# Kernel optimization log

Hardware: AMD Instinct MI355X
Metric: run time of the kernel (lower is better)

The kernel has to match this reference:

```python
import jax, jax.numpy as jnp
import numpy as np

EMBED_DIM = 1024
SEQ_LEN = 2048
BATCH = 4


def setup_inputs() -> dict:
    key = jax.random.key(0)
    kx, kq, kk, kv = jax.random.split(key, 4)
    scale = 1.0 / np.sqrt(EMBED_DIM)
    x = jax.random.normal(kx, (BATCH, SEQ_LEN, EMBED_DIM), dtype=jnp.float32)
    # nn.Linear weights are [out, in]; stored transposed-application here
    W_query = jax.random.normal(kq, (EMBED_DIM, EMBED_DIM), dtype=jnp.float32) * scale
    W_key = jax.random.normal(kk, (EMBED_DIM, EMBED_DIM), dtype=jnp.float32) * scale
    W_value = jax.random.normal(kv, (EMBED_DIM, EMBED_DIM), dtype=jnp.float32) * scale
    return {"x": x, "W_query": W_query, "W_key": W_key, "W_value": W_value}


def reference(x, W_query, W_key, W_value):
    # x: [B, S, D]; W_*: [D_out, D_in] (torch nn.Linear layout -> y = x @ W.T)
    B, S, D = x.shape
    q = jnp.einsum("bsd,ed->bse", x, W_query)
    k = jnp.einsum("bsd,ed->bse", x, W_key)
    v = jnp.einsum("bsd,ed->bse", x, W_value)
    scores = jnp.einsum("bqd,bkd->bqk", q, k)  # [B, S, S]
    causal = jnp.triu(jnp.ones((S, S), dtype=bool), k=1)  # True above diagonal
    scores = jnp.where(causal, -jnp.inf, scores)
    weights = jax.nn.softmax(scores / jnp.sqrt(jnp.asarray(D, x.dtype)), axis=-1)
    return jnp.einsum("bqk,bkd->bqd", weights, v)
```

## Files before the change

### kernel.cpp

```cpp
#include <hip/hip_runtime.h>
#include <stdint.h>

typedef __bf16 bf16_t;
typedef __bf16 bf16x8 __attribute__((ext_vector_type(8)));
typedef float  f32x4  __attribute__((ext_vector_type(4)));

#define AS1 __attribute__((address_space(1)))
#define AS3 __attribute__((address_space(3)))

__device__ __forceinline__ void gld_lds16(const bf16_t* g, void* s) {
  __builtin_amdgcn_global_load_lds((const AS1 uint32_t*)g, (AS3 uint32_t*)s, 16, 0, 0);
}

__global__ __launch_bounds__(256) void convert_all_kernel(
    const float* __restrict__ X,  const float* __restrict__ Wq,
    const float* __restrict__ Wk, const float* __restrict__ Wv,
    bf16_t* __restrict__ Xc, bf16_t* __restrict__ Wqc,
    bf16_t* __restrict__ Wkc, bf16_t* __restrict__ Wvc) {
  const int blk = blockIdx.x;
  const float* src; bf16_t* dst; int base;
  if (blk < 4096)      { src = X;  dst = Xc;  base = 0;    }
  else if (blk < 4608) { src = Wq; dst = Wqc; base = 4096; }
  else if (blk < 5120) { src = Wk; dst = Wkc; base = 4608; }
  else                 { src = Wv; dst = Wvc; base = 5120; }
  const int i = ((blk - base) * 256 + threadIdx.x) * 8;
  const float4 a = ((const float4*)(src + i))[0];
  const float4 b = ((const float4*)(src + i))[1];
  bf16x8 v;
  v[0] = (bf16_t)a.x; v[1] = (bf16_t)a.y; v[2] = (bf16_t)a.z; v[3] = (bf16_t)a.w;
  v[4] = (bf16_t)b.x; v[5] = (bf16_t)b.y; v[6] = (bf16_t)b.z; v[7] = (bf16_t)b.w;
  *(bf16x8*)(dst + i) = v;
}

__device__ __forceinline__ void gemm_bt_core(
    const bf16_t* __restrict__ A, int lda,
    const bf16_t* __restrict__ B, int ldb,
    int m0, int n0, int kBeg, int kEnd,
    bf16_t* As, bf16_t* Bs, f32x4 acc[4][4])
{
  const int tid  = threadIdx.x;
  const int lane = tid & 63;
  const int wave = tid >> 6;
  const int wm = (wave >> 1) * 64;
  const int wn = (wave & 1) * 64;
  const int fr = lane & 15;
  const int ck = lane >> 4;

  const int off0 = wave * 2048 + lane * 16;
  const int row0 = wave * 32 + (lane >> 2);
  const int row1 = row0 + 16;
  const int kg   = ((lane & 3) ^ ((row0 >> 1) & 3)) * 8;

  int aoff[4], boff[4];
#pragma unroll
  for (int i = 0; i < 4; ++i) {
    const int ra = wm + i * 16 + fr;
    const int rb = wn + i * 16 + fr;
    aoff[i] = ra * 64 + ((ck ^ ((ra >> 1) & 3)) * 16);
    boff[i] = rb * 64 + ((ck ^ ((rb >> 1) & 3)) * 16);
  }

  for (int kt = kBeg; kt < kEnd; kt += 32) {
    __syncthreads();
    gld_lds16(A + (size_t)(m0 + row0) * lda + kt + kg, (char*)As + off0);
    gld_lds16(A + (size_t)(m0 + row1) * lda + kt + kg, (char*)As + off0 + 1024);
    gld_lds16(B + (size_t)(n0 + row0) * ldb + kt + kg, (char*)Bs + off0);
    gld_lds16(B + (size_t)(n0 + row1) * ldb + kt + kg, (char*)Bs + off0 + 1024);
    __syncthreads();

    bf16x8 af[4], bfv[4];
#pragma unroll
    for (int mi = 0; mi < 4; ++mi)
      af[mi] = *(const bf16x8*)((char*)As + aoff[mi]);
#pragma unroll
    for (int ni = 0; ni < 4; ++ni)
      bfv[ni] = *(const bf16x8*)((char*)Bs + boff[ni]);
#pragma unroll
    for (int mi = 0; mi < 4; ++mi)
#pragma unroll
      for (int ni = 0; ni < 4; ++ni)
        acc[mi][ni] = __builtin_amdgcn_mfma_f32_16x16x32_bf16(
            af[mi], bfv[ni], acc[mi][ni], 0, 0, 0);
  }
}

__device__ __forceinline__ void gemm64_core(
    const bf16_t* __restrict__ A, int lda,
    const bf16_t* __restrict__ B, int ldb,
    int m0, int n0, int kBeg, int kEnd,
    bf16_t* As, bf16_t* Bs, f32x4 acc[2][2])
{
  const int lane = threadIdx.x & 63;
  const int wave = threadIdx.x >> 6;
  const int wm = (wave >> 1) * 32;
  const int wn = (wave & 1) * 32;
  const int fr = lane & 15;
  const int ck = lane >> 4;

  const int off0 = wave * 1024 + lane * 16;
  const int row0 = wave * 16 + (lane >> 2);
  const int kg   = ((lane & 3) ^ ((row0 >> 1) & 3)) * 8;

  int aoff[2], boff[2];
#pragma unroll
  for (int i = 0; i < 2; ++i) {
    const int ra = wm + i * 16 + fr;
    const int rb = wn + i * 16 + fr;
    aoff[i] = ra * 64 + ((ck ^ ((ra >> 1) & 3)) * 16);
    boff[i] = rb * 64 + ((ck ^ ((rb >> 1) & 3)) * 16);
  }

  for (int kt = kBeg; kt < kEnd; kt += 32) {
    __syncthreads();
    gld_lds16(A + (size_t)(m0 + row0) * lda + kt + kg, (char*)As + off0);
    gld_lds16(B + (size_t)(n0 + row0) * ldb + kt + kg, (char*)Bs + off0);
    __syncthreads();

    bf16x8 af[2], bfv[2];
#pragma unroll
    for (int mi = 0; mi < 2; ++mi)
      af[mi] = *(const bf16x8*)((char*)As + aoff[mi]);
#pragma unroll
    for (int ni = 0; ni < 2; ++ni)
      bfv[ni] = *(const bf16x8*)((char*)Bs + boff[ni]);
#pragma unroll
    for (int mi = 0; mi < 2; ++mi)
#pragma unroll
      for (int ni = 0; ni < 2; ++ni)
        acc[mi][ni] = __builtin_amdgcn_mfma_f32_16x16x32_bf16(
            af[mi], bfv[ni], acc[mi][ni], 0, 0, 0);
  }
}

__device__ __forceinline__ void gemm64x128_core(
    const bf16_t* __restrict__ A, int lda,
    const bf16_t* __restrict__ B, int ldb,
    int m0, int n0, int kEnd,
    bf16_t* As, bf16_t* Bs, f32x4 acc[2][4])
{
  const int lane = threadIdx.x & 63;
  const int wave = threadIdx.x >> 6;
  const int wm = (wave >> 1) * 32;
  const int wn = (wave & 1) * 64;
  const int fr = lane & 15;
  const int ck = lane >> 4;

  const int off0 = wave * 1024 + lane * 16;
  const int row0 = wave * 16 + (lane >> 2);
  const int row1 = row0 + 64;
  const int kg   = ((lane & 3) ^ ((row0 >> 1) & 3)) * 8;

  int aoff[2], boff[4];
#pragma unroll
  for (int i = 0; i < 2; ++i) {
    const int ra = wm + i * 16 + fr;
    aoff[i] = ra * 64 + ((ck ^ ((ra >> 1) & 3)) * 16);
  }
#pragma unroll
  for (int i = 0; i < 4; ++i) {
    const int rb = wn + i * 16 + fr;
    boff[i] = rb * 64 + ((ck ^ ((rb >> 1) & 3)) * 16);
  }

  for (int kt = 0; kt < kEnd; kt += 32) {
    __syncthreads();
    gld_lds16(A + (size_t)(m0 + row0) * lda + kt + kg, (char*)As + off0);
    gld_lds16(B + (size_t)(n0 + row0) * ldb + kt + kg, (char*)Bs + off0);
    gld_lds16(B + (size_t)(n0 + row1) * ldb + kt + kg, (char*)Bs + off0 + 4096);
    __syncthreads();

    bf16x8 af[2], bfv[4];
#pragma unroll
    for (int mi = 0; mi < 2; ++mi)
      af[mi] = *(const bf16x8*)((char*)As + aoff[mi]);
#pragma unroll
    for (int ni = 0; ni < 4; ++ni)
      bfv[ni] = *(const bf16x8*)((char*)Bs + boff[ni]);
#pragma unroll
    for (int mi = 0; mi < 2; ++mi)
#pragma unroll
      for (int ni = 0; ni < 4; ++ni)
        acc[mi][ni] = __builtin_amdgcn_mfma_f32_16x16x32_bf16(
            af[mi], bfv[ni], acc[mi][ni], 0, 0, 0);
  }
}

__global__ __launch_bounds__(256) void qkv_kernel(
    const bf16_t* __restrict__ X,
    const bf16_t* __restrict__ Wq, const bf16_t* __restrict__ Wk,
    const bf16_t* __restrict__ Wv,
    bf16_t* __restrict__ Q, bf16_t* __restrict__ K, bf16_t* __restrict__ V)
{
  __shared__ bf16_t As[128 * 32];
  __shared__ bf16_t Bs[128 * 32];
  const int m0 = blockIdx.x * 128;
  const int n0 = blockIdx.y * 128;
  const int z  = blockIdx.z;
  const bf16_t* W = (z == 0) ? Wq : (z == 1) ? Wk : Wv;
  bf16_t* Out     = (z == 0) ? Q  : (z == 1) ? K  : V;

  f32x4 acc[4][4] = {};
  gemm_bt_core(X, 1024, W, 1024, m0, n0, 0, 1024, As, Bs, acc);

  const int lane = threadIdx.x & 63;
  const int wave = threadIdx.x >> 6;
  const int wm = (wave >> 1) * 64, wn = (wave & 1) * 64;
#pragma unroll
  for (int mi = 0; mi < 4; ++mi)
#pragma unroll
    for (int r = 0; r < 4; ++r) {
      const int row = m0 + wm + mi * 16 + (lane >> 4) * 4 + r;
#pragma unroll
      for (int ni = 0; ni < 4; ++ni) {
        const int col = n0 + wn + ni * 16 + (lane & 15);
        Out[(size_t)row * 1024 + col] = (bf16_t)acc[mi][ni][r];
      }
    }
}

__global__ __launch_bounds__(256) void vt_kernel(
    const bf16_t* __restrict__ V, bf16_t* __restrict__ Vt)
{
  __shared__ bf16_t t[64][66];
  const int b  = blockIdx.z;
  const int s0 = blockIdx.x * 64;
  const int d0 = blockIdx.y * 64;
  const bf16_t* Vb = V  + (size_t)b * 2048 * 1024;
  bf16_t* Vtb      = Vt + (size_t)b * 1024 * 2048;
  const int c = threadIdx.x & 63, r4 = threadIdx.x >> 6;
#pragma unroll
  for (int i = 0; i < 16; ++i) {
    const int r = r4 + i * 4;
    t[r][c] = Vb[(size_t)(s0 + r) * 1024 + d0 + c];
  }
  __syncthreads();
#pragma unroll
  for (int i = 0; i < 16; ++i) {
    const int r = r4 + i * 4;
    Vtb[(size_t)(d0 + r) * 2048 + s0 + c] = t[c][r];
  }
}

__global__ __launch_bounds__(256) void scores_exp_kernel(
    const bf16_t* __restrict__ Q, const bf16_t* __restrict__ K,
    bf16_t* __restrict__ P, float* __restrict__ partials, int b0)
{
  const int kt = blockIdx.x;
  const int m0 = blockIdx.y * 64;
  const int n0 = kt * 128;
  if (n0 > m0 + 63) return;
  __shared__ bf16_t As[64 * 32];
  __shared__ bf16_t Bs[128 * 32];
  __shared__ float rowsum[2][64];
  const int batch = b0 + blockIdx.z;
  const bf16_t* Qb = Q + (size_t)batch * 2048 * 1024;
  const bf16_t* Kb = K + (size_t)batch * 2048 * 1024;
  bf16_t* Pb = P + (size_t)blockIdx.z * 2048 * 2048;
  float* lp  = partials + ((size_t)blockIdx.z * 16 + kt) * 2048;

  f32x4 acc[2][4] = {};
  gemm64x128_core(Qb, 1024, Kb, 1024, m0, n0, 1024, As, Bs, acc);

  const int lane = threadIdx.x & 63;
  const int wave = threadIdx.x >> 6;
  const int wm = (wave >> 1) * 32, wn = (wave & 1) * 64;
  const float c = 0.04508422f;
#pragma unroll
  for (int mi = 0; mi < 2; ++mi)
#pragma unroll
    for (int r = 0; r < 4; ++r) {
      const int lrow = wm + mi * 16 + (lane >> 4) * 4 + r;
      const int row  = m0 + lrow;
      float rs = 0.f;
#pragma unroll
      for (int ni = 0; ni < 4; ++ni) {
        const int col = n0 + wn + ni * 16 + (lane & 15);
        float p = exp2f(acc[mi][ni][r] * c);
        if (col > row) p = 0.f;
        const bf16_t pb = (bf16_t)p;
        Pb[(size_t)row * 2048 + col] = pb;
        rs += (float)pb;
      }
      rs += __shfl_xor(rs, 1);
      rs += __shfl_xor(rs, 2);
      rs += __shfl_xor(rs, 4);
      rs += __shfl_xor(rs, 8);
      if ((lane & 15) == 0) rowsum[wave & 1][lrow] = rs;
    }
  __syncthreads();
  if (threadIdx.x < 64)
    lp[m0 + threadIdx.x] = rowsum[0][threadIdx.x] + rowsum[1][threadIdx.x];
}

__global__ __launch_bounds__(256) void pv_kernel(
    const bf16_t* __restrict__ P, const bf16_t* __restrict__ Vt,
    const float* __restrict__ partials, float* __restrict__ out, int b0)
{
  __shared__ bf16_t As[64 * 32];
  __shared__ bf16_t Bs[64 * 32];
  const int n0   = blockIdx.x * 64;
  const int pair = blockIdx.y;
  const int batch = b0 + blockIdx.z;
  const bf16_t* Pb  = P  + (size_t)blockIdx.z * 2048 * 2048;
  const bf16_t* Vtb = Vt + (size_t)batch * 1024 * 2048;
  const float* lp = partials + (size_t)blockIdx.z * 16 * 2048;
  float* ob = out + (size_t)batch * 2048 * 1024;

  const int lane = threadIdx.x & 63;
  const int wave = threadIdx.x >> 6;
  const int wm = (wave >> 1) * 32, wn = (wave & 1) * 32;

#pragma unroll
  for (int t = 0; t < 2; ++t) {
    const int mt = t ? (31 - pair) : pair;
    const int m0 = mt * 64;
    const int kEnd = m0 + 64;

    f32x4 acc[2][2] = {};
    gemm64_core(Pb, 2048, Vtb, 2048, m0, n0, 0, kEnd, As, Bs, acc);

#pragma unroll
    for (int mi = 0; mi < 2; ++mi)
#pragma unroll
      for (int r = 0; r < 4; ++r) {
        const int row = m0 + wm + mi * 16 + (lane >> 4) * 4 + r;
        const int tmax = row >> 7;
        float l = 0.f;
        for (int kt = 0; kt <= tmax; ++kt) l += lp[kt * 2048 + row];
        const float inv = 1.f / l;
#pragma unroll
        for (int ni = 0; ni < 2; ++ni) {
          const int col = n0 + wn + ni * 16 + (lane & 15);
          ob[(size_t)row * 1024 + col] = acc[mi][ni][r] * inv;
        }
      }
  }
}

extern "C" void kernel_launch(void* const* d_in, const int* in_sizes, int n_in,
                              void* d_out, int out_size, void* d_ws, size_t ws_size,
                              hipStream_t stream) {
  const float* X  = (const float*)d_in[0];
  const float* Wq = (const float*)d_in[1];
  const float* Wk = (const float*)d_in[2];
  const float* Wv = (const float*)d_in[3];
  float* out = (float*)d_out;
  char* ws = (char*)d_ws;

  const size_t NX = (size_t)4 * 2048 * 1024;
  const size_t NW = (size_t)1024 * 1024;
  const size_t QKV_BYTES = NX * 2;

  size_t  off  = 0;
  bf16_t* Xc   = (bf16_t*)(ws + off); off += NX * 2;
  bf16_t* Wqc  = (bf16_t*)(ws + off); off += NW * 2;
  bf16_t* Wkc  = (bf16_t*)(ws + off); off += NW * 2;
  bf16_t* Wvc  = (bf16_t*)(ws + off); off += NW * 2;
  bf16_t* Q    = (bf16_t*)(ws + off); off += QKV_BYTES;
  bf16_t* K    = (bf16_t*)(ws + off); off += QKV_BYTES;
  bf16_t* V    = (bf16_t*)(ws + off); off += QKV_BYTES;
  bf16_t* Vt   = (bf16_t*)(ws + off); off += QKV_BYTES;

  const size_t L_B = (size_t)16 * 2048 * 4;
  const size_t P_B = (size_t)2048 * 2048 * 2;
  const int NB = (ws_size >= off + 4 * (L_B + P_B)) ? 4 : 1;
  float*  Lp = (float*)(ws + off);
  bf16_t* Pb = (bf16_t*)(ws + off + (size_t)NB * L_B);

  convert_all_kernel<<<dim3(5632), 256, 0, stream>>>(X, Wq, Wk, Wv, Xc, Wqc, Wkc, Wvc);
  qkv_kernel<<<dim3(64, 8, 3), 256, 0, stream>>>(Xc, Wqc, Wkc, Wvc, Q, K, V);
  vt_kernel<<<dim3(32, 16, 4), 256, 0, stream>>>(V, Vt);
  for (int b0 = 0; b0 < 4; b0 += NB) {
    scores_exp_kernel<<<dim3(16, 32, NB), 256, 0, stream>>>(Q, K, Pb, Lp, b0);
    pv_kernel<<<dim3(16, 16, NB), 256, 0, stream>>>(Pb, Vt, Lp, out, b0);
  }
}
```

Measured before the change: 268.8 us.

## Use 128x128 tiles in PV GEMM and precompute inverse row sums

The PV kernel moves from 64x64 tiles with paired causal rows to 128x128 tiles using the existing gemm_bt_core, with a per-batch rotation of the row-tile order. A separate small kernel sums the per-tile partial row sums once and stores reciprocals in the reused Wqc buffer, so the epilogue no longer repeats the partial-sum loop in every block. Larger tiles raise data reuse and MFMA density per LDS load. The cost is that the causal work imbalance is no longer hidden by pairing, and there are fewer blocks plus one extra launch.

```diff
diff --git a/kernel.cpp b/kernel.cpp
--- a/kernel.cpp
+++ b/kernel.cpp
@@ -84,54 +84,6 @@
   }
 }
 
-__device__ __forceinline__ void gemm64_core(
-    const bf16_t* __restrict__ A, int lda,
-    const bf16_t* __restrict__ B, int ldb,
-    int m0, int n0, int kBeg, int kEnd,
-    bf16_t* As, bf16_t* Bs, f32x4 acc[2][2])
-{
-  const int lane = threadIdx.x & 63;
-  const int wave = threadIdx.x >> 6;
-  const int wm = (wave >> 1) * 32;
-  const int wn = (wave & 1) * 32;
-  const int fr = lane & 15;
-  const int ck = lane >> 4;
-
-  const int off0 = wave * 1024 + lane * 16;
-  const int row0 = wave * 16 + (lane >> 2);
-  const int kg   = ((lane & 3) ^ ((row0 >> 1) & 3)) * 8;
-
-  int aoff[2], boff[2];
-#pragma unroll
-  for (int i = 0; i < 2; ++i) {
-    const int ra = wm + i * 16 + fr;
-    const int rb = wn + i * 16 + fr;
-    aoff[i] = ra * 64 + ((ck ^ ((ra >> 1) & 3)) * 16);
-    boff[i] = rb * 64 + ((ck ^ ((rb >> 1) & 3)) * 16);
-  }
-
-  for (int kt = kBeg; kt < kEnd; kt += 32) {
-    __syncthreads();
-    gld_lds16(A + (size_t)(m0 + row0) * lda + kt + kg, (char*)As + off0);
-    gld_lds16(B + (size_t)(n0 + row0) * ldb + kt + kg, (char*)Bs + off0);
-    __syncthreads();
-
-    bf16x8 af[2], bfv[2];
-#pragma unroll
-    for (int mi = 0; mi < 2; ++mi)
-      af[mi] = *(const bf16x8*)((char*)As + aoff[mi]);
-#pragma unroll
-    for (int ni = 0; ni < 2; ++ni)
-      bfv[ni] = *(const bf16x8*)((char*)Bs + boff[ni]);
-#pragma unroll
-    for (int mi = 0; mi < 2; ++mi)
-#pragma unroll
-      for (int ni = 0; ni < 2; ++ni)
-        acc[mi][ni] = __builtin_amdgcn_mfma_f32_16x16x32_bf16(
-            af[mi], bfv[ni], acc[mi][ni], 0, 0, 0);
-  }
-}
-
 __device__ __forceinline__ void gemm64x128_core(
     const bf16_t* __restrict__ A, int lda,
     const bf16_t* __restrict__ B, int ldb,
@@ -292,49 +244,53 @@
     lp[m0 + threadIdx.x] = rowsum[0][threadIdx.x] + rowsum[1][threadIdx.x];
 }
 
+__global__ __launch_bounds__(256) void lsum_kernel(
+    const float* __restrict__ partials, float* __restrict__ Linv)
+{
+  const int id  = blockIdx.x * 256 + threadIdx.x;
+  const int z   = id >> 11;
+  const int row = id & 2047;
+  const float* lp = partials + (size_t)z * 16 * 2048;
+  const int tmax = row >> 7;
+  float l = 0.f;
+  for (int kt = 0; kt <= tmax; ++kt) l += lp[kt * 2048 + row];
+  Linv[id] = 1.f / l;
+}
+
 __global__ __launch_bounds__(256) void pv_kernel(
     const bf16_t* __restrict__ P, const bf16_t* __restrict__ Vt,
-    const float* __restrict__ partials, float* __restrict__ out, int b0)
-{
-  __shared__ bf16_t As[64 * 32];
-  __shared__ bf16_t Bs[64 * 32];
-  const int n0   = blockIdx.x * 64;
-  const int pair = blockIdx.y;
-  const int batch = b0 + blockIdx.z;
-  const bf16_t* Pb  = P  + (size_t)blockIdx.z * 2048 * 2048;
+    const float* __restrict__ Linv, float* __restrict__ out, int b0)
+{
+  __shared__ bf16_t As[128 * 32];
+  __shared__ bf16_t Bs[128 * 32];
+  const int zb = blockIdx.z;
+  const int mt = (blockIdx.y + 5 * zb) & 15;
+  const int m0 = mt * 128;
+  const int n0 = blockIdx.x * 128;
+  const int batch = b0 + zb;
+  const bf16_t* Pb  = P  + (size_t)zb * 2048 * 2048;
   const bf16_t* Vtb = Vt + (size_t)batch * 1024 * 2048;
-  const float* lp = partials + (size_t)blockIdx.z * 16 * 2048;
+  const float* li = Linv + (size_t)zb * 2048;
   float* ob = out + (size_t)batch * 2048 * 1024;
+
+  f32x4 acc[4][4] = {};
+  gemm_bt_core(Pb, 2048, Vtb, 2048, m0, n0, 0, m0 + 128, As, Bs, acc);
 
   const int lane = threadIdx.x & 63;
   const int wave = threadIdx.x >> 6;
-  const int wm = (wave >> 1) * 32, wn = (wave & 1) * 32;
-
-#pragma unroll
-  for (int t = 0; t < 2; ++t) {
-    const int mt = t ? (31 - pair) : pair;
-    const int m0 = mt * 64;
-    const int kEnd = m0 + 64;
-
-    f32x4 acc[2][2] = {};
-    gemm64_core(Pb, 2048, Vtb, 2048, m0, n0, 0, kEnd, As, Bs, acc);
-
-#pragma unroll
-    for (int mi = 0; mi < 2; ++mi)
-#pragma unroll
-      for (int r = 0; r < 4; ++r) {
-        const int row = m0 + wm + mi * 16 + (lane >> 4) * 4 + r;
-        const int tmax = row >> 7;
-        float l = 0.f;
-        for (int kt = 0; kt <= tmax; ++kt) l += lp[kt * 2048 + row];
-        const float inv = 1.f / l;
-#pragma unroll
-        for (int ni = 0; ni < 2; ++ni) {
-          const int col = n0 + wn + ni * 16 + (lane & 15);
-          ob[(size_t)row * 1024 + col] = acc[mi][ni][r] * inv;
-        }
+  const int wm = (wave >> 1) * 64, wn = (wave & 1) * 64;
+#pragma unroll
+  for (int mi = 0; mi < 4; ++mi)
+#pragma unroll
+    for (int r = 0; r < 4; ++r) {
+      const int row = m0 + wm + mi * 16 + (lane >> 4) * 4 + r;
+      const float inv = li[row];
+#pragma unroll
+      for (int ni = 0; ni < 4; ++ni) {
+        const int col = n0 + wn + ni * 16 + (lane & 15);
+        ob[(size_t)row * 1024 + col] = acc[mi][ni][r] * inv;
       }
-  }
+    }
 }
 
 extern "C" void kernel_launch(void* const* d_in, const int* in_sizes, int n_in,
@@ -361,6 +317,8 @@
   bf16_t* V    = (bf16_t*)(ws + off); off += QKV_BYTES;
   bf16_t* Vt   = (bf16_t*)(ws + off); off += QKV_BYTES;
 
+  float* Linv = (float*)Wqc;
+
   const size_t L_B = (size_t)16 * 2048 * 4;
   const size_t P_B = (size_t)2048 * 2048 * 2;
   const int NB = (ws_size >= off + 4 * (L_B + P_B)) ? 4 : 1;
@@ -372,6 +330,7 @@
   vt_kernel<<<dim3(32, 16, 4), 256, 0, stream>>>(V, Vt);
   for (int b0 = 0; b0 < 4; b0 += NB) {
     scores_exp_kernel<<<dim3(16, 32, NB), 256, 0, stream>>>(Q, K, Pb, Lp, b0);
-    pv_kernel<<<dim3(16, 16, NB), 256, 0, stream>>>(Pb, Vt, Lp, out, b0);
-  }
-}
+    lsum_kernel<<<dim3(NB * 8), 256, 0, stream>>>(Lp, Linv);
+    pv_kernel<<<dim3(8, 16, NB), 256, 0, stream>>>(Pb, Vt, Linv, out, b0);
+  }
+}
```

New measurement: 260.1 us. 1.03x faster.
